# Optimization experiments

Hardware: AMD Instinct MI355X
Metric: run time of the kernel (lower is better)

The kernel has to match this reference:

```python
import jax, jax.numpy as jnp
import numpy as np

B, T, D, H, L = 8, 150, 30, 5, 3
HD = D // H  # 6
ORIG = (300, 74, 35)


def setup_inputs() -> dict:
    key = jax.random.key(0)
    ks = iter(jax.random.split(key, 40))
    def g(shape, s=0.05):
        return jax.random.normal(next(ks), shape, dtype=jnp.float32) * s
    return {
        "x_l": g((B, T, ORIG[0]), 1.0),
        "x_a": g((B, T, ORIG[1]), 1.0),
        "x_v": g((B, T, ORIG[2]), 1.0),
        "Wl": g((D, ORIG[0])),
        "Wa": g((D, ORIG[1])),
        "Wv": g((D, ORIG[2])),
        "in_w": g((2, L, 3 * D, D)),
        "in_b": jnp.zeros((2, L, 3 * D), jnp.float32),
        "out_w": g((2, L, D, D)),
        "out_b": jnp.zeros((2, L, D), jnp.float32),
        "lin1_w": g((2, L, 4 * D, D)),
        "lin1_b": jnp.zeros((2, L, 4 * D), jnp.float32),
        "lin2_w": g((2, L, D, 4 * D)),
        "lin2_b": jnp.zeros((2, L, D), jnp.float32),
        "n1_g": jnp.ones((2, L, D), jnp.float32),
        "n1_b": jnp.zeros((2, L, D), jnp.float32),
        "n2_g": jnp.ones((2, L, D), jnp.float32),
        "n2_b": jnp.zeros((2, L, D), jnp.float32),
        "p1_w": g((2 * D, 2 * D)),
        "p1_b": jnp.zeros((2 * D,), jnp.float32),
        "p2_w": g((2 * D, 2 * D)),
        "p2_b": jnp.zeros((2 * D,), jnp.float32),
        "ow": g((1, 2 * D)),
        "ob": jnp.zeros((1,), jnp.float32),
    }


def _ln(x, g, b, eps=1e-5):
    m = x.mean(-1, keepdims=True)
    v = jnp.var(x, axis=-1, keepdims=True)  # biased var, matches torch LayerNorm
    return (x - m) * jax.lax.rsqrt(v + eps) * g + b


def _heads(x):  # [Tt, B, D] -> [B*H, Tt, HD]
    Tt = x.shape[0]
    return x.reshape(Tt, B * H, HD).transpose(1, 0, 2)


def _layer(x, xk, xv, p):
    iw, ib, ow, ob, w1, b1, w2, b2, g1, bb1, g2, bb2 = p
    res = x
    xn, kn, vn = _ln(x, g1, bb1), _ln(xk, g1, bb1), _ln(xv, g1, bb1)
    q = (xn @ iw[:D].T + ib[:D]) * (HD ** -0.5)
    k = kn @ iw[D:2 * D].T + ib[D:2 * D]
    v = vn @ iw[2 * D:].T + ib[2 * D:]
    qh, kh, vh = _heads(q), _heads(k), _heads(v)
    # trilinear scores: [B*H, Tq, Tk, Tv]
    aw = jnp.einsum('iat,ibt,ict->iabc', qh, kh, vh)
    fused = aw.mean(-1) + aw.max(-1)          # fuse over value axis -> [B*H, Tq, Tk]
    fused = jax.nn.softmax(fused, axis=-1)
    attn = jnp.einsum('iab,ibt->iat', fused, qh)  # NB: original bmm uses q, not v
    attn = attn.transpose(1, 0, 2).reshape(-1, B, D)
    x = res + (attn @ ow.T + ob)
    res = x
    xn = _ln(x, g2, bb2)
    x = jax.nn.relu(xn @ w1.T + b1) @ w2.T + b2
    return res + x


def reference(x_l, x_a, x_v, Wl, Wa, Wv, in_w, in_b, out_w, out_b,
              lin1_w, lin1_b, lin2_w, lin2_b, n1_g, n1_b, n2_g, n2_b,
              p1_w, p1_b, p2_w, p2_b, ow, ob):
    pl = (x_l @ Wl.T).transpose(1, 0, 2)  # [T, B, D] (conv1d k=1, no bias)
    pa = (x_a @ Wa.T).transpose(1, 0, 2)
    pv = (x_v @ Wv.T).transpose(1, 0, 2)
    hs = []
    for s, (kk, vv) in enumerate(((pa, pv), (pv, pa))):
        h = pl
        for l in range(L):
            p = (in_w[s, l], in_b[s, l], out_w[s, l], out_b[s, l],
                 lin1_w[s, l], lin1_b[s, l], lin2_w[s, l], lin2_b[s, l],
                 n1_g[s, l], n1_b[s, l], n2_g[s, l], n2_b[s, l])
            h = _layer(h, kk, vv, p)
        hs.append(h[-1])  # last timestep [B, D]
    last_hs = jnp.concatenate(hs, axis=1)  # [B, 2D]
    proj = jax.nn.relu(last_hs @ p1_w.T + p1_b) @ p2_w.T + p2_b + last_hs
    out = proj @ ow.T + ob
    return (out, last_hs)
```

## Files before the change

kernel.cpp:

```cpp
#include <hip/hip_runtime.h>
#include <math.h>

#define BB 8
#define TT 150
#define DD 30
#define HH 5
#define HD 6
#define LL 3
#define NI 40
#define ROWF (TT*BB*DD)
#define RSTR 8
#define NR 152

typedef _Float16 half8 __attribute__((ext_vector_type(8)));
typedef float f32x16 __attribute__((ext_vector_type(16)));

__device__ __forceinline__ float wsum(float v) {
    #pragma unroll
    for (int m = 32; m > 0; m >>= 1) v += __shfl_xor(v, m, 64);
    return v;
}

__device__ __forceinline__ float max3f(float a, float b, float c) {
    return fmaxf(fmaxf(a, b), c);
}

__global__ __launch_bounds__(256) void projkvq_kernel(
    const float* __restrict__ x_l, const float* __restrict__ x_a, const float* __restrict__ x_v,
    const float* __restrict__ Wl, const float* __restrict__ Wa, const float* __restrict__ Wv,
    const float* __restrict__ in_w, const float* __restrict__ in_b,
    const float* __restrict__ n1g, const float* __restrict__ n1b,
    float* __restrict__ pl,
    _Float16* __restrict__ k_all, _Float16* __restrict__ v_all, _Float16* __restrict__ q) {
    int blk = blockIdx.x;
    int tid = threadIdx.x;
    int w = tid >> 6, lane = tid & 63;
    int tb = blk * 4 + w;
    int t = tb / BB, b = tb % BB;

    __shared__ float WS[30 * 301];
    __shared__ float xl[4][304];
    __shared__ float xa[4][80];
    __shared__ float xv[4][40];
    __shared__ float rrow[3][4][32];
    __shared__ float dco[4][3][32];
    __shared__ float xkv[4][2][32];
    __shared__ float xq[4][32];

    const float* xpl = x_l + ((size_t)b * TT + t) * 300;
    const float* xpa = x_a + ((size_t)b * TT + t) * 74;
    const float* xpv = x_v + ((size_t)b * TT + t) * 35;
    for (int j = lane; j < 300; j += 64) xl[w][j] = xpl[j];
    for (int j = lane; j < 74; j += 64) xa[w][j] = xpa[j];
    if (lane < 35) xv[w][lane] = xpv[lane];

    int d = lane >> 1, jh = lane & 1;
    int dc = d < DD ? d : 0;
    float accL, accA, accV;

    for (int j = tid; j < 9000; j += 256) WS[(j / 300) * 301 + (j % 300)] = Wl[j];
    __syncthreads();
    {
        const float* wr = WS + (size_t)dc * 301;
        int j0 = jh ? 150 : 0, j1 = jh ? 300 : 150;
        float acc = 0.f;
        for (int j = j0; j < j1; j++) acc += xl[w][j] * wr[j];
        acc += __shfl_xor(acc, 1, 64);
        accL = acc;
    }
    __syncthreads();
    for (int j = tid; j < 2220; j += 256) WS[(j / 74) * 75 + (j % 74)] = Wa[j];
    __syncthreads();
    {
        const float* wr = WS + (size_t)dc * 75;
        int j0 = jh ? 37 : 0, j1 = jh ? 74 : 37;
        float acc = 0.f;
        for (int j = j0; j < j1; j++) acc += xa[w][j] * wr[j];
        acc += __shfl_xor(acc, 1, 64);
        accA = acc;
    }
    __syncthreads();
    for (int j = tid; j < 1050; j += 256) WS[j] = Wv[j];
    __syncthreads();
    {
        const float* wr = WS + (size_t)dc * 35;
        int j0 = jh ? 17 : 0, j1 = jh ? 35 : 17;
        float acc = 0.f;
        for (int j = j0; j < j1; j++) acc += xv[w][j] * wr[j];
        acc += __shfl_xor(acc, 1, 64);
        accV = acc;
    }
    if (jh == 0 && d < DD) {
        pl[t * (BB * DD) + b * DD + d] = accL;
        rrow[0][w][d] = accL;
        rrow[1][w][d] = accA;
        rrow[2][w][d] = accV;
    }
    __syncthreads();

    #pragma unroll
    for (int src = 0; src < 3; src++) {
        float xval = (lane < 30) ? rrow[src][w][lane] : 0.f;
        float mean = wsum(xval) * (1.f / 30.f);
        float dv = (lane < 30) ? (xval - mean) : 0.f;
        float var = wsum(dv * dv) * (1.f / 30.f);
        float inv = rsqrtf(var + 1e-5f);
        if (lane < 30) dco[w][src][lane] = dv * inv;
    }
    __syncthreads();

    for (int po = 0; po < 6; po++) {
        int s = po / LL;
        int kin = (s == 0) ? 1 : 2;
        int vin = (s == 0) ? 2 : 1;
        const float* g = n1g + (size_t)po * 30;
        const float* bb = n1b + (size_t)po * 30;
        for (int j = tid; j < 1800; j += 256) WS[j] = in_w[(size_t)po * 2700 + 900 + j];
        int half = lane >> 5, dd2 = lane & 31;
        if (dd2 < 30) {
            int sel = half ? vin : kin;
            xkv[w][half][dd2] = dco[w][sel][dd2] * g[dd2] + bb[dd2];
        }
        __syncthreads();
        if (lane < 60) {
            int which = lane / 30, dd = lane % 30;
            const float* wr = WS + lane * 30;
            float acc = 0.f;
            #pragma unroll 6
            for (int j = 0; j < 30; j++) acc += wr[j] * xkv[w][which][j];
            acc += in_b[po * 90 + 30 + lane];
            int i = b * HH + dd / HD, hd = dd % HD;
            _Float16* dst = which ? v_all : k_all;
            size_t row = (((size_t)po * NI + i) * TT + t) * 8;
            dst[row + hd] = (_Float16)acc;
            if (hd < 2) dst[row + 6 + hd] = (_Float16)0.f;
        }
        __syncthreads();
    }

    for (int s2 = 0; s2 < 2; s2++) {
        int po = s2 * LL;
        const float* g = n1g + (size_t)po * 30;
        const float* bb = n1b + (size_t)po * 30;
        for (int j = tid; j < 900; j += 256) WS[j] = in_w[(size_t)po * 2700 + j];
        if (lane < 30) xq[w][lane] = dco[w][0][lane] * g[lane] + bb[lane];
        __syncthreads();
        if (lane < 30) {
            const float* wr = WS + lane * 30;
            float acc = 0.f;
            #pragma unroll 6
            for (int j = 0; j < 30; j++) acc += wr[j] * xq[w][j];
            acc = (acc + in_b[po * 90 + lane]) * 0.40824829046386307f;
            int i = b * HH + lane / HD, hd = lane % HD;
            size_t rw = (((size_t)s2 * NI + i) * TT + t) * 8;
            q[rw + hd] = (_Float16)acc;
            if (hd < 2) q[rw + 6 + hd] = (_Float16)0.f;
        }
        __syncthreads();
    }
}

__global__ __launch_bounds__(256, 4) void score_kernel(
    const _Float16* __restrict__ q, const _Float16* __restrict__ k_all,
    const _Float16* __restrict__ v_all, int l, float* __restrict__ attn) {
    int blk = blockIdx.x;
    int s = blk / 760;
    int rem = blk % 760;
    int i = rem / 19;
    int g = rem % 19;
    int tid = threadIdx.x;
    int wv = tid >> 6, lane = tid & 63;
    int lo = lane & 31, hf = lane >> 5;
    int po = s * LL + l;

    __shared__ __align__(16) _Float16 qsh[NR * RSTR];
    __shared__ __align__(16) _Float16 ksh[NR * RSTR];
    __shared__ __align__(16) _Float16 vsh[NR * RSTR];

    const _Float16* qg = q + (size_t)(s * NI + i) * TT * 8;
    const _Float16* kg = k_all + ((size_t)po * NI + i) * TT * 8;
    const _Float16* vg = v_all + ((size_t)po * NI + i) * TT * 8;
    half8 z8;
    #pragma unroll
    for (int t = 0; t < 8; t++) z8[t] = (_Float16)0.f;
    for (int r = tid; r < NR; r += 256) {
        half8 qa = z8, ka = z8, va = z8;
        if (r < TT) {
            qa = *(const half8*)&qg[r * 8];
            ka = *(const half8*)&kg[r * 8];
            va = *(const half8*)&vg[r * 8];
        }
        *(half8*)&qsh[r * RSTR] = qa;
        *(half8*)&ksh[r * RSTR] = ka;
        *(half8*)&vsh[r * RSTR] = va;
    }
    __syncthreads();
    if (wv == 0) {
        float v6[6] = {0.f, 0.f, 0.f, 0.f, 0.f, 0.f};
        for (int c = lane; c < TT; c += 64) {
            #pragma unroll
            for (int t = 0; t < 6; t++) v6[t] += (float)vsh[c * RSTR + t];
        }
        #pragma unroll
        for (int m = 32; m > 0; m >>= 1) {
            #pragma unroll
            for (int t = 0; t < 6; t++) v6[t] += __shfl_xor(v6[t], m, 64);
        }
        if (lane < 6) vsh[TT * RSTR + lane] = (_Float16)(v6[lane] * (1.f / TT));
    }
    __syncthreads();

    f32x16 zacc;
    #pragma unroll
    for (int j = 0; j < 16; j++) zacc[j] = 0.f;

    half8 bfrag[5], vhalf[5];
    #pragma unroll
    for (int nt = 0; nt < 5; nt++) {
        int rr = nt * 32 + lo;
        int rc = rr < 151 ? rr : 151;
        half8 kf = *(const half8*)&ksh[rc * RSTR];
        half8 vf = *(const half8*)&vsh[rc * RSTR];
        bfrag[nt] = hf ? z8 : kf;
        vhalf[nt] = hf ? z8 : vf;
    }

    for (int ap = 0; ap < 2; ap++) {
        int a = g * 8 + wv * 2 + ap;
        if (a >= TT) break;
        half8 qav = *(const half8*)&qsh[a * RSTR];
        half8 afrag[5];
        #pragma unroll
        for (int nt = 0; nt < 5; nt++) afrag[nt] = vhalf[nt] * qav;

        float fsc[5];
        #pragma unroll
        for (int nb = 0; nb < 5; nb++) {
            float tm[4];
            #pragma unroll
            for (int ma = 0; ma < 4; ma++) {
                f32x16 acc = __builtin_amdgcn_mfma_f32_32x32x16_f16(afrag[ma], bfrag[nb], zacc, 0, 0, 0);
                float u0 = max3f(acc[0], acc[1], acc[2]);
                float u1 = max3f(acc[3], acc[4], acc[5]);
                float u2 = max3f(acc[6], acc[7], acc[8]);
                float u3 = max3f(acc[9], acc[10], acc[11]);
                float u4 = max3f(acc[12], acc[13], acc[14]);
                tm[ma] = fmaxf(max3f(u0, u1, u2), max3f(u3, u4, acc[15]));
            }
            f32x16 a4 = __builtin_amdgcn_mfma_f32_32x32x16_f16(afrag[4], bfrag[nb], zacc, 0, 0, 0);
            float t0 = max3f(a4[0], a4[1], a4[2]);
            float t1 = max3f(a4[3], a4[4], a4[5]);
            float t2 = max3f(a4[6], a4[7], a4[8]);
            float ext = (hf == 0) ? fmaxf(a4[10], a4[11]) : -INFINITY;
            float rest = fmaxf(a4[9], ext);
            float m4 = fmaxf(max3f(t0, t1, t2), rest);
            float rm = fmaxf(max3f(tm[0], tm[1], tm[2]), fmaxf(tm[3], m4));
            float om = __shfl_xor(a4[10], 32, 64);
            float mn = hf ? a4[10] : om;
            rm = fmaxf(rm, __shfl_xor(rm, 32, 64));
            int bcol = nb * 32 + lo;
            fsc[nb] = (bcol < TT) ? (mn + rm) : -INFINITY;
        }
        float m = fmaxf(max3f(fsc[0], fsc[1], fsc[2]), fmaxf(fsc[3], fsc[4]));
        #pragma unroll
        for (int msk = 16; msk > 0; msk >>= 1) m = fmaxf(m, __shfl_xor(m, msk, 64));
        float e[5], es = 0.f;
        #pragma unroll
        for (int nb = 0; nb < 5; nb++) { e[nb] = __expf(fsc[nb] - m); es += e[nb]; }
        float acc7[7] = {0.f, 0.f, 0.f, 0.f, 0.f, 0.f, 0.f};
        acc7[6] = es;
        #pragma unroll
        for (int nb = 0; nb < 5; nb++) {
            int bcol = nb * 32 + lo;
            int bi = (bcol < TT) ? bcol : 0;
            float wgt = e[nb];
            half8 qrow = *(const half8*)&qsh[bi * RSTR];
            #pragma unroll
            for (int t = 0; t < 6; t++) acc7[t] += wgt * (float)qrow[t];
        }
        #pragma unroll
        for (int msk = 16; msk > 0; msk >>= 1) {
            #pragma unroll
            for (int t = 0; t < 7; t++) acc7[t] += __shfl_xor(acc7[t], msk, 64);
        }
        if (lane == 0) {
            float inv = 1.f / acc7[6];
            int bo = i / HH, ho = i % HH;
            float* dst = attn + (size_t)s * ROWF + a * (BB * DD) + bo * DD + ho * HD;
            #pragma unroll
            for (int t = 0; t < 6; t++) dst[t] = acc7[t] * inv;
        }
    }
}

__global__ __launch_bounds__(256) void ffnlnq_kernel(
    const float* __restrict__ attn, const float* __restrict__ pl,
    const float* __restrict__ out_w, const float* __restrict__ out_b,
    const float* __restrict__ l1w, const float* __restrict__ l1b,
    const float* __restrict__ l2w, const float* __restrict__ l2b,
    const float* __restrict__ n2g, const float* __restrict__ n2b,
    const float* __restrict__ in_w, const float* __restrict__ in_b,
    const float* __restrict__ n1g, const float* __restrict__ n1b,
    int l, int has_next,
    float* __restrict__ h, _Float16* __restrict__ q) {
    int blk = blockIdx.x;
    int s = blk / 300;
    int w = threadIdx.x >> 6, lane = threadIdx.x & 63;
    int tb = (blk % 300) * 4 + w;
    int t = tb / BB, b = tb % BB;
    int po = s * LL + l;
    const float* ow = out_w + (size_t)po * 900;
    const float* ob = out_b + (size_t)po * 30;
    const float* w1 = l1w + (size_t)po * 3600;
    const float* b1 = l1b + (size_t)po * 120;
    const float* w2 = l2w + (size_t)po * 3600;
    const float* b2 = l2b + (size_t)po * 30;
    const float* g2 = n2g + (size_t)po * 30;
    const float* bb2 = n2b + (size_t)po * 30;
    __shared__ float owS[900];
    __shared__ float w1T[30 * 128];
    __shared__ float w2S[30 * 121];
    __shared__ float iwqS[900];
    __shared__ float arS[4][30], xnS[4][32], hidS[4][120], xqS[4][30];
    for (int j = threadIdx.x; j < 900; j += 256) owS[j] = ow[j];
    for (int j = threadIdx.x; j < 3600; j += 256) w1T[(j % 30) * 128 + (j / 30)] = w1[j];
    for (int j = threadIdx.x; j < 3600; j += 256) w2S[(j / 120) * 121 + (j % 120)] = w2[j];
    if (has_next) {
        const float* iwq = in_w + (size_t)(po + 1) * 2700;
        for (int j = threadIdx.x; j < 900; j += 256) iwqS[j] = iwq[j];
    }
    __syncthreads();
    float* hrow = h + (size_t)s * ROWF + (size_t)tb * 30;
    const float* res = (l == 0) ? (pl + (size_t)tb * 30) : hrow;
    const float* arow = attn + (size_t)s * ROWF + (size_t)tb * 30;
    if (lane < 30) arS[w][lane] = arow[lane];
    float x1v = 0.f;
    if (lane < 30) {
        const float* wr = owS + lane * 30;
        float acc = 0.f;
        #pragma unroll 6
        for (int j = 0; j < 30; j++) acc += wr[j] * arS[w][j];
        x1v = res[lane] + acc + ob[lane];
    }
    float mean = wsum(x1v) * (1.f / 30.f);
    float dv = (lane < 30) ? (x1v - mean) : 0.f;
    float var = wsum(dv * dv) * (1.f / 30.f);
    float inv = rsqrtf(var + 1e-5f);
    if (lane < 30) xnS[w][lane] = dv * inv * g2[lane] + bb2[lane];
    for (int o = lane; o < 120; o += 64) {
        float acc = 0.f;
        #pragma unroll 6
        for (int j = 0; j < 30; j++) acc += w1T[j * 128 + o] * xnS[w][j];
        hidS[w][o] = fmaxf(acc + b1[o], 0.f);
    }
    float newh = 0.f;
    if (lane < 30) {
        const float* wr = w2S + lane * 121;
        float acc = 0.f;
        #pragma unroll 8
        for (int j = 0; j < 120; j++) acc += wr[j] * hidS[w][j];
        newh = x1v + acc + b2[lane];
        hrow[lane] = newh;
    }
    if (has_next) {
        const float* g1 = n1g + (size_t)(po + 1) * 30;
        const float* bb1 = n1b + (size_t)(po + 1) * 30;
        const float* ibq = in_b + (size_t)(po + 1) * 90;
        float mean2 = wsum(newh) * (1.f / 30.f);
        float dv2 = (lane < 30) ? (newh - mean2) : 0.f;
        float var2 = wsum(dv2 * dv2) * (1.f / 30.f);
        float inv2 = rsqrtf(var2 + 1e-5f);
        if (lane < 30) xqS[w][lane] = dv2 * inv2 * g1[lane] + bb1[lane];
        if (lane < 30) {
            const float* wr = iwqS + lane * 30;
            float acc = 0.f;
            #pragma unroll 6
            for (int j = 0; j < 30; j++) acc += wr[j] * xqS[w][j];
            acc = (acc + ibq[lane]) * 0.40824829046386307f;
            int i = b * HH + lane / HD, hd = lane % HD;
            size_t rw = (((size_t)s * NI + i) * TT + t) * 8;
            q[rw + hd] = (_Float16)acc;
            if (hd < 2) q[rw + 6 + hd] = (_Float16)0.f;
        }
    }
}

__global__ __launch_bounds__(256) void head_kernel(
    const float* __restrict__ h,
    const float* __restrict__ p1w, const float* __restrict__ p1b,
    const float* __restrict__ p2w, const float* __restrict__ p2b,
    const float* __restrict__ ow, const float* __restrict__ ob,
    float* __restrict__ out) {
    int tid = threadIdx.x;
    __shared__ float lh[480], hid[480], pr[480];
    for (int idx = tid; idx < 480; idx += 256) {
        int b = idx / 60, j = idx % 60;
        int s = j / 30, d = j % 30;
        float vv = h[(size_t)s * ROWF + 149 * (BB * DD) + b * DD + d];
        lh[idx] = vv;
        out[8 + idx] = vv;
    }
    __syncthreads();
    for (int idx = tid; idx < 480; idx += 256) {
        int b = idx / 60, o = idx % 60;
        const float* wr = p1w + o * 60;
        float acc = p1b[o];
        for (int j = 0; j < 60; j++) acc += wr[j] * lh[b * 60 + j];
        hid[idx] = fmaxf(acc, 0.f);
    }
    __syncthreads();
    for (int idx = tid; idx < 480; idx += 256) {
        int b = idx / 60, d = idx % 60;
        const float* wr = p2w + d * 60;
        float acc = p2b[d];
        for (int j = 0; j < 60; j++) acc += wr[j] * hid[b * 60 + j];
        pr[idx] = acc + lh[idx];
    }
    __syncthreads();
    if (tid < 8) {
        float acc = ob[0];
        for (int j = 0; j < 60; j++) acc += pr[tid * 60 + j] * ow[j];
        out[tid] = acc;
    }
}

extern "C" void kernel_launch(void* const* d_in, const int* in_sizes, int n_in,
                              void* d_out, int out_size, void* d_ws, size_t ws_size,
                              hipStream_t stream) {
    const float* x_l   = (const float*)d_in[0];
    const float* x_a   = (const float*)d_in[1];
    const float* x_v   = (const float*)d_in[2];
    const float* Wl    = (const float*)d_in[3];
    const float* Wa    = (const float*)d_in[4];
    const float* Wv    = (const float*)d_in[5];
    const float* in_w  = (const float*)d_in[6];
    const float* in_b  = (const float*)d_in[7];
    const float* out_w = (const float*)d_in[8];
    const float* out_b = (const float*)d_in[9];
    const float* l1w   = (const float*)d_in[10];
    const float* l1b   = (const float*)d_in[11];
    const float* l2w   = (const float*)d_in[12];
    const float* l2b   = (const float*)d_in[13];
    const float* n1g   = (const float*)d_in[14];
    const float* n1b   = (const float*)d_in[15];
    const float* n2g   = (const float*)d_in[16];
    const float* n2b   = (const float*)d_in[17];
    const float* p1w   = (const float*)d_in[18];
    const float* p1b   = (const float*)d_in[19];
    const float* p2w   = (const float*)d_in[20];
    const float* p2b   = (const float*)d_in[21];
    const float* oww   = (const float*)d_in[22];
    const float* obb   = (const float*)d_in[23];

    float* ws = (float*)d_ws;
    float* pl    = ws;
    float* h     = ws + 36000;
    float* at    = ws + 108000;
    _Float16* qh = (_Float16*)(ws + 180000);
    _Float16* kh = (_Float16*)(ws + 228000);
    _Float16* vh = (_Float16*)(ws + 372000);

    projkvq_kernel<<<300, 256, 0, stream>>>(x_l, x_a, x_v, Wl, Wa, Wv,
                                            in_w, in_b, n1g, n1b,
                                            pl, kh, vh, qh);
    for (int l = 0; l < LL; l++) {
        score_kernel<<<1520, 256, 0, stream>>>(qh, kh, vh, l, at);
        ffnlnq_kernel<<<600, 256, 0, stream>>>(at, pl, out_w, out_b, l1w, l1b, l2w, l2b,
                                               n2g, n2b, in_w, in_b, n1g, n1b,
                                               l, (l < LL - 1) ? 1 : 0, h, qh);
    }
    head_kernel<<<1, 256, 0, stream>>>(h, p1w, p1b, p2w, p2b, oww, obb, (float*)d_out);
}
```

Before: 243.1 us.

## Split front projection kernel across per-layer blocks and parallelize FFN second matmul

The single 300-block projection kernel that looped over six layer/stream K/V projections and two Q projections is replaced by a 2400-block kernel. Each block handles one (layer, row-group) K/V projection or one stream's Q projection, which raises parallelism and uses a smaller shared-memory footprint through a union. The cost is redundant recomputation of the input projections (Wa, Wv, Wl) in many blocks. Separately, the FFN second matmul now splits each output's 120-long dot product across two lanes and combines them with shuffles, so 60 lanes work instead of 30.

```diff
diff --git a/kernel.cpp b/kernel.cpp
--- a/kernel.cpp
+++ b/kernel.cpp
@@ -25,7 +25,15 @@
     return fmaxf(fmaxf(a, b), c);
 }
 
-__global__ __launch_bounds__(256) void projkvq_kernel(
+union FMem {
+    struct { float WaS[2250]; float WvS[1050]; float iwS[1800];
+             float xa[4][80]; float xv[4][40];
+             float rr[2][4][32]; float xn[4][2][32]; } kv;
+    struct { float Wc[30 * 151]; float iwS[900]; float xl[4][304];
+             float rr[4][32]; float xn[4][32]; } qp;
+};
+
+__global__ __launch_bounds__(256) void front_kernel(
     const float* __restrict__ x_l, const float* __restrict__ x_a, const float* __restrict__ x_v,
     const float* __restrict__ Wl, const float* __restrict__ Wa, const float* __restrict__ Wv,
     const float* __restrict__ in_w, const float* __restrict__ in_b,
@@ -35,99 +43,60 @@
     int blk = blockIdx.x;
     int tid = threadIdx.x;
     int w = tid >> 6, lane = tid & 63;
-    int tb = blk * 4 + w;
-    int t = tb / BB, b = tb % BB;
-
-    __shared__ float WS[30 * 301];
-    __shared__ float xl[4][304];
-    __shared__ float xa[4][80];
-    __shared__ float xv[4][40];
-    __shared__ float rrow[3][4][32];
-    __shared__ float dco[4][3][32];
-    __shared__ float xkv[4][2][32];
-    __shared__ float xq[4][32];
-
-    const float* xpl = x_l + ((size_t)b * TT + t) * 300;
-    const float* xpa = x_a + ((size_t)b * TT + t) * 74;
-    const float* xpv = x_v + ((size_t)b * TT + t) * 35;
-    for (int j = lane; j < 300; j += 64) xl[w][j] = xpl[j];
-    for (int j = lane; j < 74; j += 64) xa[w][j] = xpa[j];
-    if (lane < 35) xv[w][lane] = xpv[lane];
-
-    int d = lane >> 1, jh = lane & 1;
-    int dc = d < DD ? d : 0;
-    float accL, accA, accV;
-
-    for (int j = tid; j < 9000; j += 256) WS[(j / 300) * 301 + (j % 300)] = Wl[j];
-    __syncthreads();
-    {
-        const float* wr = WS + (size_t)dc * 301;
-        int j0 = jh ? 150 : 0, j1 = jh ? 300 : 150;
-        float acc = 0.f;
-        for (int j = j0; j < j1; j++) acc += xl[w][j] * wr[j];
-        acc += __shfl_xor(acc, 1, 64);
-        accL = acc;
-    }
-    __syncthreads();
-    for (int j = tid; j < 2220; j += 256) WS[(j / 74) * 75 + (j % 74)] = Wa[j];
-    __syncthreads();
-    {
-        const float* wr = WS + (size_t)dc * 75;
-        int j0 = jh ? 37 : 0, j1 = jh ? 74 : 37;
-        float acc = 0.f;
-        for (int j = j0; j < j1; j++) acc += xa[w][j] * wr[j];
-        acc += __shfl_xor(acc, 1, 64);
-        accA = acc;
-    }
-    __syncthreads();
-    for (int j = tid; j < 1050; j += 256) WS[j] = Wv[j];
-    __syncthreads();
-    {
-        const float* wr = WS + (size_t)dc * 35;
-        int j0 = jh ? 17 : 0, j1 = jh ? 35 : 17;
-        float acc = 0.f;
-        for (int j = j0; j < j1; j++) acc += xv[w][j] * wr[j];
-        acc += __shfl_xor(acc, 1, 64);
-        accV = acc;
-    }
-    if (jh == 0 && d < DD) {
-        pl[t * (BB * DD) + b * DD + d] = accL;
-        rrow[0][w][d] = accL;
-        rrow[1][w][d] = accA;
-        rrow[2][w][d] = accV;
-    }
-    __syncthreads();
-
-    #pragma unroll
-    for (int src = 0; src < 3; src++) {
-        float xval = (lane < 30) ? rrow[src][w][lane] : 0.f;
-        float mean = wsum(xval) * (1.f / 30.f);
-        float dv = (lane < 30) ? (xval - mean) : 0.f;
-        float var = wsum(dv * dv) * (1.f / 30.f);
-        float inv = rsqrtf(var + 1e-5f);
-        if (lane < 30) dco[w][src][lane] = dv * inv;
-    }
-    __syncthreads();
-
-    for (int po = 0; po < 6; po++) {
+    __shared__ FMem sm;
+
+    if (blk < 1800) {
+        int po = blk / 300;
         int s = po / LL;
-        int kin = (s == 0) ? 1 : 2;
-        int vin = (s == 0) ? 2 : 1;
-        const float* g = n1g + (size_t)po * 30;
+        int tb = (blk % 300) * 4 + w;
+        int t = tb / BB, b = tb % BB;
+        for (int j = tid; j < 2220; j += 256) sm.kv.WaS[(j / 74) * 75 + (j % 74)] = Wa[j];
+        for (int j = tid; j < 1050; j += 256) sm.kv.WvS[j] = Wv[j];
+        for (int j = tid; j < 1800; j += 256) sm.kv.iwS[j] = in_w[(size_t)po * 2700 + 900 + j];
+        const float* xpa = x_a + ((size_t)b * TT + t) * 74;
+        const float* xpv = x_v + ((size_t)b * TT + t) * 35;
+        for (int j = lane; j < 74; j += 64) sm.kv.xa[w][j] = xpa[j];
+        if (lane < 35) sm.kv.xv[w][lane] = xpv[lane];
+        __syncthreads();
+        int d = lane >> 1, jh = lane & 1;
+        int dc = d < DD ? d : 0;
+        {
+            const float* wr = sm.kv.WaS + dc * 75;
+            int j0 = jh ? 37 : 0, j1 = jh ? 74 : 37;
+            float acc = 0.f;
+            for (int j = j0; j < j1; j++) acc += sm.kv.xa[w][j] * wr[j];
+            acc += __shfl_xor(acc, 1, 64);
+            if (jh == 0 && d < DD) sm.kv.rr[0][w][d] = acc;
+        }
+        {
+            const float* wr = sm.kv.WvS + dc * 35;
+            int j0 = jh ? 17 : 0, j1 = jh ? 35 : 17;
+            float acc = 0.f;
+            for (int j = j0; j < j1; j++) acc += sm.kv.xv[w][j] * wr[j];
+            acc += __shfl_xor(acc, 1, 64);
+            if (jh == 0 && d < DD) sm.kv.rr[1][w][d] = acc;
+        }
+        __syncthreads();
+        const float* g  = n1g + (size_t)po * 30;
         const float* bb = n1b + (size_t)po * 30;
-        for (int j = tid; j < 1800; j += 256) WS[j] = in_w[(size_t)po * 2700 + 900 + j];
-        int half = lane >> 5, dd2 = lane & 31;
-        if (dd2 < 30) {
-            int sel = half ? vin : kin;
-            xkv[w][half][dd2] = dco[w][sel][dd2] * g[dd2] + bb[dd2];
+        int sel0 = (s == 0) ? 0 : 1;
+        for (int r = 0; r < 2; r++) {
+            int src = (r == 0) ? sel0 : (1 - sel0);
+            float xval = (lane < 30) ? sm.kv.rr[src][w][lane] : 0.f;
+            float mean = wsum(xval) * (1.f / 30.f);
+            float dv = (lane < 30) ? (xval - mean) : 0.f;
+            float var = wsum(dv * dv) * (1.f / 30.f);
+            float inv = rsqrtf(var + 1e-5f);
+            if (lane < 30) sm.kv.xn[w][r][lane] = dv * inv * g[lane] + bb[lane];
         }
         __syncthreads();
         if (lane < 60) {
             int which = lane / 30, dd = lane % 30;
-            const float* wr = WS + lane * 30;
+            const float* wr = sm.kv.iwS + lane * 30;
+            const float* xv2 = sm.kv.xn[w][which];
             float acc = 0.f;
             #pragma unroll 6
-            for (int j = 0; j < 30; j++) acc += wr[j] * xkv[w][which][j];
+            for (int j = 0; j < 30; j++) acc += wr[j] * xv2[j];
             acc += in_b[po * 90 + 30 + lane];
             int i = b * HH + dd / HD, hd = dd % HD;
             _Float16* dst = which ? v_all : k_all;
@@ -135,28 +104,57 @@
             dst[row + hd] = (_Float16)acc;
             if (hd < 2) dst[row + 6 + hd] = (_Float16)0.f;
         }
-        __syncthreads();
-    }
-
-    for (int s2 = 0; s2 < 2; s2++) {
-        int po = s2 * LL;
-        const float* g = n1g + (size_t)po * 30;
+    } else {
+        int r2 = blk - 1800;
+        int s = r2 / 300;
+        int tb = (r2 % 300) * 4 + w;
+        int t = tb / BB, b = tb % BB;
+        int po = s * LL;
+        for (int j = tid; j < 900; j += 256) sm.qp.iwS[j] = in_w[(size_t)po * 2700 + j];
+        const float* xpl = x_l + ((size_t)b * TT + t) * 300;
+        for (int j = lane; j < 300; j += 64) sm.qp.xl[w][j] = xpl[j];
+        for (int j = tid; j < 4500; j += 256)
+            sm.qp.Wc[(j / 150) * 151 + (j % 150)] = Wl[(size_t)(j / 150) * 300 + (j % 150)];
+        __syncthreads();
+        int d = lane >> 1, jh = lane & 1;
+        int dc = d < DD ? d : 0;
+        float acc = 0.f;
+        if (jh == 0) {
+            const float* wr = sm.qp.Wc + dc * 151;
+            for (int j = 0; j < 150; j++) acc += sm.qp.xl[w][j] * wr[j];
+        }
+        __syncthreads();
+        for (int j = tid; j < 4500; j += 256)
+            sm.qp.Wc[(j / 150) * 151 + (j % 150)] = Wl[(size_t)(j / 150) * 300 + 150 + (j % 150)];
+        __syncthreads();
+        if (jh == 1) {
+            const float* wr = sm.qp.Wc + dc * 151;
+            for (int j = 0; j < 150; j++) acc += sm.qp.xl[w][150 + j] * wr[j];
+        }
+        acc += __shfl_xor(acc, 1, 64);
+        if (jh == 0 && d < DD) {
+            if (s == 0) pl[t * (BB * DD) + b * DD + d] = acc;
+            sm.qp.rr[w][d] = acc;
+        }
+        const float* g  = n1g + (size_t)po * 30;
         const float* bb = n1b + (size_t)po * 30;
-        for (int j = tid; j < 900; j += 256) WS[j] = in_w[(size_t)po * 2700 + j];
-        if (lane < 30) xq[w][lane] = dco[w][0][lane] * g[lane] + bb[lane];
-        __syncthreads();
+        float xval = (lane < 30) ? sm.qp.rr[w][lane] : 0.f;
+        float mean = wsum(xval) * (1.f / 30.f);
+        float dv = (lane < 30) ? (xval - mean) : 0.f;
+        float var = wsum(dv * dv) * (1.f / 30.f);
+        float inv = rsqrtf(var + 1e-5f);
+        if (lane < 30) sm.qp.xn[w][lane] = dv * inv * g[lane] + bb[lane];
         if (lane < 30) {
-            const float* wr = WS + lane * 30;
-            float acc = 0.f;
+            const float* wr = sm.qp.iwS + lane * 30;
+            float acc2 = 0.f;
             #pragma unroll 6
-            for (int j = 0; j < 30; j++) acc += wr[j] * xq[w][j];
-            acc = (acc + in_b[po * 90 + lane]) * 0.40824829046386307f;
+            for (int j = 0; j < 30; j++) acc2 += wr[j] * sm.qp.xn[w][j];
+            acc2 = (acc2 + in_b[po * 90 + lane]) * 0.40824829046386307f;
             int i = b * HH + lane / HD, hd = lane % HD;
-            size_t rw = (((size_t)s2 * NI + i) * TT + t) * 8;
-            q[rw + hd] = (_Float16)acc;
+            size_t rw = (((size_t)s * NI + i) * TT + t) * 8;
+            q[rw + hd] = (_Float16)acc2;
             if (hd < 2) q[rw + 6 + hd] = (_Float16)0.f;
         }
-        __syncthreads();
     }
 }
 
@@ -353,13 +351,20 @@
         for (int j = 0; j < 30; j++) acc += w1T[j * 128 + o] * xnS[w][j];
         hidS[w][o] = fmaxf(acc + b1[o], 0.f);
     }
+    float acc2p = 0.f;
+    if (lane < 60) {
+        int d2 = lane >> 1, part = lane & 1;
+        const float* wr = w2S + d2 * 121;
+        int j0 = part ? 60 : 0, j1 = part ? 120 : 60;
+        #pragma unroll 6
+        for (int j = j0; j < j1; j++) acc2p += wr[j] * hidS[w][j];
+        acc2p += __shfl_xor(acc2p, 1, 64);
+    }
+    int srcl = (lane < 30) ? (lane << 1) : 0;
+    float accG = __shfl(acc2p, srcl, 64);
     float newh = 0.f;
     if (lane < 30) {
-        const float* wr = w2S + lane * 121;
-        float acc = 0.f;
-        #pragma unroll 8
-        for (int j = 0; j < 120; j++) acc += wr[j] * hidS[w][j];
-        newh = x1v + acc + b2[lane];
+        newh = x1v + accG + b2[lane];
         hrow[lane] = newh;
     }
     if (has_next) {
@@ -460,9 +465,9 @@
     _Float16* kh = (_Float16*)(ws + 228000);
     _Float16* vh = (_Float16*)(ws + 372000);
 
-    projkvq_kernel<<<300, 256, 0, stream>>>(x_l, x_a, x_v, Wl, Wa, Wv,
-                                            in_w, in_b, n1g, n1b,
-                                            pl, kh, vh, qh);
+    front_kernel<<<2400, 256, 0, stream>>>(x_l, x_a, x_v, Wl, Wa, Wv,
+                                           in_w, in_b, n1g, n1b,
+                                           pl, kh, vh, qh);
     for (int l = 0; l < LL; l++) {
         score_kernel<<<1520, 256, 0, stream>>>(qh, kh, vh, l, at);
         ffnlnq_kernel<<<600, 256, 0, stream>>>(at, pl, out_w, out_b, l1w, l1b, l2w, l2b,
```

After: 242.3 us. Within noise of the previous version (-0.4%).
